# Performance work log

Measured on AMD Instinct MI355X. Metric: run time of the kernel, lower is better.

## Reference

```python
import jax, jax.numpy as jnp
import numpy as np

N = 20000      # nodes
E = 320000     # edges per timestep
T = 16         # timesteps
F_IN = 128     # node_features
F1, H1 = 64, 4 # gat1 filters/heads (concat=True)
F2, H2 = 64, 4 # gat2 filters/heads (concat=False -> mean over heads)
NEG_SLOPE = 0.2
EPS = 1e-16


def setup_inputs() -> dict:
    key = jax.random.key(0)
    ks = jax.random.split(key, 18)
    s = 0.05
    rn = lambda k, shp: (jax.random.normal(k, shp, jnp.float32) * s)
    return {
        "x_sequence": jax.random.normal(ks[0], (N, T, F_IN), jnp.float32),
        "edge_index_sequence": jax.random.randint(ks[1], (T, 2, E), 0, N, jnp.int32),
        # GATConv 1 (in=F_IN, out=F1, heads=H1, concat=True)
        "W1": rn(ks[2], (F_IN, H1 * F1)),
        "att_src1": rn(ks[3], (H1, F1)),
        "att_dst1": rn(ks[4], (H1, F1)),
        "b1": rn(ks[5], (H1 * F1,)),
        # GATConv 2 (in=H1*F1, out=F2, heads=H2, concat=False)
        "W2": rn(ks[6], (H1 * F1, H2 * F2)),
        "att_src2": rn(ks[7], (H2, F2)),
        "att_dst2": rn(ks[8], (H2, F2)),
        "b2": rn(ks[9], (F2,)),
        # GRU (input=F2, hidden=F2); layout: x @ W_ih + b_ih, gates [r|z|n]
        "W_ih": rn(ks[10], (F2, 3 * F2)),
        "W_hh": rn(ks[11], (F2, 3 * F2)),
        "b_ih": rn(ks[12], (3 * F2,)),
        "b_hh": rn(ks[13], (3 * F2,)),
        # final Linear(F2 -> 1)
        "W_out": rn(ks[14], (F2, 1)),
        "b_out": rn(ks[15], (1,)),
    }


def _gat(x, src, dst, W, a_src, a_dst, bias, heads, out_ch, concat):
    """PyG-style GATConv with self-loops already appended to (src, dst)."""
    n = x.shape[0]
    h = (x @ W).reshape(n, heads, out_ch)            # [N, H, C]
    al_src = jnp.einsum("nhc,hc->nh", h, a_src)       # [N, H]
    al_dst = jnp.einsum("nhc,hc->nh", h, a_dst)
    e = al_src[src] + al_dst[dst]                     # [E, H]
    e = jax.nn.leaky_relu(e, NEG_SLOPE)
    # segment softmax over edges grouped by destination node
    m = jax.ops.segment_max(e, dst, num_segments=n)   # [N, H]
    e = jnp.exp(e - m[dst])
    denom = jax.ops.segment_sum(e, dst, num_segments=n)
    alpha = e / (denom[dst] + EPS)                    # [E, H]
    msg = h[src] * alpha[:, :, None]                  # [E, H, C]
    out = jax.ops.segment_sum(msg, dst, num_segments=n)  # [N, H, C]
    out = out.reshape(n, heads * out_ch) if concat else out.mean(axis=1)
    return out + bias


def reference(x_sequence, edge_index_sequence, W1, att_src1, att_dst1, b1,
              W2, att_src2, att_dst2, b2, W_ih, W_hh, b_ih, b_hh, W_out, b_out):
    loops = jnp.arange(N, dtype=edge_index_sequence.dtype)

    def gat_step(_, inp):
        x_t, ei = inp                                 # [N,F_IN], [2,E]
        src = jnp.concatenate([ei[0], loops])         # add self-loops
        dst = jnp.concatenate([ei[1], loops])
        h = jax.nn.relu(_gat(x_t, src, dst, W1, att_src1, att_dst1, b1, H1, F1, True))
        h = jax.nn.relu(_gat(h, src, dst, W2, att_src2, att_dst2, b2, H2, F2, False))
        return None, h

    xs = (jnp.swapaxes(x_sequence, 0, 1), edge_index_sequence)  # [T,N,F_IN], [T,2,E]
    _, gat_out = jax.lax.scan(gat_step, None, xs)               # [T, N, F2]

    def gru_step(h_prev, x_t):
        gi = x_t @ W_ih + b_ih
        gh = h_prev @ W_hh + b_hh
        ir, iz, ig = jnp.split(gi, 3, axis=-1)
        hr, hz, hg = jnp.split(gh, 3, axis=-1)
        r = jax.nn.sigmoid(ir + hr)
        z = jax.nn.sigmoid(iz + hz)
        g = jnp.tanh(ig + r * hg)
        h = (1.0 - z) * g + z * h_prev
        return h, None

    h0 = jnp.zeros((N, F2), x_sequence.dtype)
    h_last, _ = jax.lax.scan(gru_step, h0, gat_out)             # [N, F2]
    return (h_last @ W_out + b_out).squeeze(-1)                  # [N]
```

## Files before the change

### kernel.cpp

```cpp
#include <hip/hip_runtime.h>
#include <math.h>

#define N_NODES 20000
#define N_EDGES 320000
#define T_STEPS 16
#define TB 8
#define RB_ROWS (N_NODES * TB)
#define F_INDIM 128
#define HC 256
#define HEADS 4
#define CDIM 64
#define G3 192
#define EPN (N_EDGES + N_NODES)
#define CSR_NB 20
#define CSR_EPB 16000

typedef __attribute__((ext_vector_type(8))) short bf16x8;
typedef __attribute__((ext_vector_type(8))) unsigned short ushort8;
typedef __attribute__((ext_vector_type(4))) float f32x4;
typedef __attribute__((ext_vector_type(4))) _Float16 half4;
typedef __attribute__((ext_vector_type(8))) _Float16 half8;

__device__ inline unsigned short f2bf(float x) {
    unsigned int u = __builtin_bit_cast(unsigned int, x);
    u += 0x7fffu + ((u >> 16) & 1u);
    return (unsigned short)(u >> 16);
}
__device__ inline void split_hilo(float x, unsigned short& h, unsigned short& l) {
    h = f2bf(x);
    float hf = __builtin_bit_cast(float, (unsigned int)h << 16);
    l = f2bf(x - hf);
}
__device__ inline ushort8 f4_to_hilo(float4 v) {
    ushort8 o;
    split_hilo(v.x, ((unsigned short*)&o)[0], ((unsigned short*)&o)[1]);
    split_hilo(v.y, ((unsigned short*)&o)[2], ((unsigned short*)&o)[3]);
    split_hilo(v.z, ((unsigned short*)&o)[4], ((unsigned short*)&o)[5]);
    split_hilo(v.w, ((unsigned short*)&o)[6], ((unsigned short*)&o)[7]);
    return o;
}
__device__ inline float fsig(float x) { return 1.f / (1.f + __expf(-x)); }
__device__ inline float ftanh(float x) {
    x = fminf(fmaxf(x, -15.f), 15.f);
    float e = __expf(2.f * x);
    return (e - 1.f) / (e + 1.f);
}


__global__ void k_wsplit(const float* __restrict__ W, unsigned short* __restrict__ Wt,
                         int K, int Ncol) {
    int idx = blockIdx.x * 256 + threadIdx.x;
    if (idx >= K * Ncol) return;
    int k = idx / Ncol, c = idx - k * Ncol;
    unsigned short h, l;
    split_hilo(W[idx], h, l);
    Wt[(size_t)c * 2 * K + 2 * k] = h;
    Wt[(size_t)c * 2 * K + 2 * k + 1] = l;
}

__global__ void k_whalf(const float* __restrict__ W, _Float16* __restrict__ Wt,
                        int K, int Ncol) {
    int idx = blockIdx.x * 256 + threadIdx.x;
    if (idx >= K * Ncol) return;
    int k = idx / Ncol, c = idx - k * Ncol;
    Wt[(size_t)c * K + k] = (_Float16)W[idx];
}


__global__ __launch_bounds__(1024) void k_csr_hist(const int* __restrict__ ei,
                                                   unsigned int* __restrict__ partial,
                                                   unsigned short* __restrict__ lrank16) {
    __shared__ unsigned int hist[N_NODES];
    const int t = blockIdx.y, b = blockIdx.x;
    const int tid = threadIdx.x;
    for (int i = tid; i < N_NODES; i += 1024) hist[i] = 0;
    __syncthreads();
    const int* dst = ei + (size_t)t * 2 * N_EDGES + N_EDGES;
    const int e1 = min(b * CSR_EPB + CSR_EPB, N_EDGES);
    for (int e = b * CSR_EPB + tid; e < e1; e += 1024) {
        unsigned int lr = atomicAdd(&hist[dst[e]], 1u);
        lrank16[(size_t)t * N_EDGES + e] = (unsigned short)lr;
    }
    __syncthreads();
    unsigned int* pp = partial + ((size_t)t * CSR_NB + b) * N_NODES;
    for (int i = tid; i < N_NODES; i += 1024) pp[i] = hist[i];
}

__global__ void k_csr_colscan(unsigned int* __restrict__ partial,
                              unsigned int* __restrict__ total) {
    int idx = blockIdx.x * 256 + threadIdx.x;
    if (idx >= T_STEPS * N_NODES) return;
    int t = idx / N_NODES;
    int d = idx - t * N_NODES;
    unsigned int* pb = partial + (size_t)t * CSR_NB * N_NODES + d;
    unsigned int acc = 0;
#pragma unroll
    for (int b = 0; b < CSR_NB; ++b) {
        unsigned int c = pb[(size_t)b * N_NODES];
        pb[(size_t)b * N_NODES] = acc;
        acc += c;
    }
    total[idx] = acc + 1;
}

__global__ __launch_bounds__(1024) void k_csr_scan(const unsigned int* __restrict__ total,
                                                   int* __restrict__ off_all,
                                                   unsigned short* __restrict__ csr16) {
    __shared__ int sdata[1024];
    const int t = blockIdx.x;
    const unsigned int* tot = total + (size_t)t * N_NODES;
    int* off = off_all + t * (N_NODES + 1);
    unsigned short* cs = csr16 + (size_t)t * EPN;
    const int tid = threadIdx.x;
    const int ITEMS = (N_NODES + 1023) / 1024;
    const int start = tid * ITEMS;
    int local = 0;
    for (int i = 0; i < ITEMS; ++i) {
        int d = start + i;
        if (d < N_NODES) local += tot[d];
    }
    sdata[tid] = local;
    __syncthreads();
    for (int s = 1; s < 1024; s <<= 1) {
        int v = (tid >= s) ? sdata[tid - s] : 0;
        __syncthreads();
        sdata[tid] += v;
        __syncthreads();
    }
    int run = sdata[tid] - local;
    for (int i = 0; i < ITEMS; ++i) {
        int d = start + i;
        if (d < N_NODES) {
            off[d] = run;
            cs[run] = (unsigned short)d;
            run += tot[d];
        }
    }
    if (tid == 0) off[N_NODES] = EPN;
}

__global__ void k_csr_fold(unsigned int* __restrict__ partial,
                           const int* __restrict__ off_all) {
    int idx = blockIdx.x * 256 + threadIdx.x;
    if (idx >= T_STEPS * CSR_NB * N_NODES) return;
    int t = idx / (CSR_NB * N_NODES);
    int rem = idx - t * (CSR_NB * N_NODES);
    int d = rem % N_NODES;
    partial[idx] += (unsigned int)(off_all[t * (N_NODES + 1) + d] + 1);
}

__global__ void k_csr_fill(const int* __restrict__ ei,
                           const unsigned int* __restrict__ partial,
                           const unsigned short* __restrict__ lrank16,
                           unsigned short* __restrict__ csr16) {
    const int bid = blockIdx.x;
    const int t = bid & 15;
    const int i = bid >> 4;
    const int e = i * 256 + threadIdx.x;
    const int* ep = ei + (size_t)t * 2 * N_EDGES;
    int s = ep[e], d = ep[N_EDGES + e];
    int b = e / CSR_EPB;
    unsigned int pos = partial[((size_t)t * CSR_NB + b) * N_NODES + d]
                     + lrank16[(size_t)t * N_EDGES + e];
    csr16[(size_t)t * EPN + pos] = (unsigned short)s;
}


template <bool XMAP, bool ATTN, bool CHALF, int BN, bool AF32, int DT>
__global__ __launch_bounds__(256) void k_gemm_mfma(const unsigned short* __restrict__ A, int lda,
                                                   const unsigned short* __restrict__ Bt,
                                                   float* __restrict__ C, int ldc,
                                                   int K2, int tbase,
                                                   const float* __restrict__ a_src,
                                                   const float* __restrict__ a_dst,
                                                   float* __restrict__ asb,
                                                   float* __restrict__ adb) {
    __shared__ unsigned short sA[128][40];
    __shared__ unsigned short sB[BN][40];
    const int NJ = BN / 16;
    const int tid = threadIdx.x;
    const int wid = tid >> 6, lane = tid & 63;
    const int row0 = blockIdx.y * 128;
    const int col0 = blockIdx.x * BN;

    const int ar = tid >> 1, aq = (tid & 1) * 8;
    const int bc = tid >> 2, bq = (tid & 3) * 8;

    int l = row0 + ar;
    int rg;
    if (XMAP) { int tl = l / N_NODES; int s = l - tl * N_NODES; rg = s * T_STEPS + tbase + tl; }
    else rg = l;
    const unsigned short* Arow = A + (size_t)rg * lda;
    const float* Arowf = (const float*)A + (size_t)rg * lda;
    const unsigned short* Brow = Bt + (size_t)(col0 + bc) * K2;
    const unsigned short* Brow2 = (BN == 128) ? (Bt + (size_t)(col0 + bc + 64) * K2) : Brow;

    const int fr = lane & 15;
    const int kg = lane >> 4;

    f32x4 acc[2][NJ] = {};

    for (int kk = 0; kk < K2; kk += 32) {
        ushort8 a0, a1;
        if (AF32) {
            float4 fa0 = *(const float4*)(Arowf + ((kk + aq) >> 1));
            float4 fa1 = *(const float4*)(Arowf + ((kk + aq) >> 1) + 8);
            a0 = f4_to_hilo(fa0);
            a1 = f4_to_hilo(fa1);
        } else {
            a0 = *(const ushort8*)(Arow + kk + aq);
            a1 = *(const ushort8*)(Arow + kk + aq + 16);
        }
        ushort8 b0 = *(const ushort8*)(Brow + kk + bq);
        ushort8 b1;
        if (BN == 128) b1 = *(const ushort8*)(Brow2 + kk + bq);
        *(ushort8*)&sA[ar][aq] = a0;
        *(ushort8*)&sA[ar][aq + 16] = a1;
        *(ushort8*)&sB[bc][bq] = b0;
        if (BN == 128) *(ushort8*)&sB[bc + 64][bq] = b1;
        __syncthreads();
        bf16x8 af[2], bfv[NJ];
#pragma unroll
        for (int i = 0; i < 2; ++i)
            af[i] = *(const bf16x8*)&sA[wid * 32 + i * 16 + fr][kg * 8];
#pragma unroll
        for (int j = 0; j < NJ; ++j)
            bfv[j] = *(const bf16x8*)&sB[j * 16 + fr][kg * 8];
#pragma unroll
        for (int i = 0; i < 2; ++i)
#pragma unroll
            for (int j = 0; j < NJ; ++j) {
                if (DT == 0)
                    acc[i][j] = __builtin_amdgcn_mfma_f32_16x16x32_bf16(af[i], bfv[j],
                                                                        acc[i][j], 0, 0, 0);
                else
                    acc[i][j] = __builtin_amdgcn_mfma_f32_16x16x32_f16(
                        __builtin_bit_cast(half8, af[i]), __builtin_bit_cast(half8, bfv[j]),
                        acc[i][j], 0, 0, 0);
            }
        __syncthreads();
    }
#pragma unroll
    for (int i = 0; i < 2; ++i)
#pragma unroll
        for (int j = 0; j < NJ; ++j) {
            int col = col0 + j * 16 + fr;
#pragma unroll
            for (int r = 0; r < 4; ++r) {
                int row = row0 + wid * 32 + i * 16 + kg * 4 + r;
                if (CHALF) {
                    _Float16* Ch = (_Float16*)C;
                    Ch[(size_t)row * ldc + col] = (_Float16)acc[i][j][r];
                } else {
                    C[(size_t)row * ldc + col] = acc[i][j][r];
                }
            }
        }

    if (ATTN) {
#pragma unroll
        for (int half = 0; half < BN / 64; ++half) {
            const int h_idx = (col0 >> 6) + half;
            float wa[4], wb[4];
#pragma unroll
            for (int j = 0; j < 4; ++j) {
                wa[j] = a_src[h_idx * 64 + j * 16 + fr];
                wb[j] = a_dst[h_idx * 64 + j * 16 + fr];
            }
#pragma unroll
            for (int i = 0; i < 2; ++i)
#pragma unroll
                for (int r = 0; r < 4; ++r) {
                    float sa = 0.f, sd = 0.f;
#pragma unroll
                    for (int j = 0; j < 4; ++j) {
                        sa = fmaf(acc[i][half * 4 + j][r], wa[j], sa);
                        sd = fmaf(acc[i][half * 4 + j][r], wb[j], sd);
                    }
#pragma unroll
                    for (int s = 1; s <= 8; s <<= 1) {
                        sa += __shfl_xor(sa, s, 64);
                        sd += __shfl_xor(sd, s, 64);
                    }
                    if (fr == 0) {
                        int row = row0 + wid * 32 + i * 16 + kg * 4 + r;
                        asb[(size_t)row * 4 + h_idx] = sa;
                        adb[(size_t)row * 4 + h_idx] = sd;
                    }
                }
        }
    }
}


template <bool CONCAT>
__global__ __launch_bounds__(256) void k_agg(const _Float16* __restrict__ hfeat,
                                             const float* __restrict__ asb,
                                             const float* __restrict__ adb,
                                             const int* __restrict__ off_all,
                                             const unsigned short* __restrict__ csr16,
                                             const float* __restrict__ bias,
                                             _Float16* __restrict__ out, int tbase) {
    const int bid = blockIdx.x;
    const int tl = bid & 7;
    const int nb = bid >> 3;
    const int t = tbase + tl;
    const int wid = threadIdx.x >> 6;
    const int d = nb * 4 + wid;
    const int lane = threadIdx.x & 63;
    const int h = lane >> 4;
    const int e16 = lane & 15;
    const int* off = off_all + (size_t)t * (N_NODES + 1);
    const int beg = off[d];
    const int deg = off[d + 1] - beg;
    const unsigned short* cs = csr16 + (size_t)t * EPN + beg;
    const float* asl = asb + (size_t)tl * N_NODES * HEADS;
    const half4* feat = (const half4*)(hfeat + (size_t)tl * N_NODES * HC) + lane;
    const float adh = adb[((size_t)tl * N_NODES + d) * HEADS + h];

    float ax = 0.f, ay = 0.f, az = 0.f, aw = 0.f, dlane = 0.f;
    const int widx = (lane & 48);

    int sreg = 0;
    float araw = 0.f;
    if (e16 < deg) {
        sreg = cs[e16];
        araw = asl[sreg * 4 + h];
    }

    for (int base = 0; base < deg; base += 16) {
        float wme = 0.f;
        if (base + e16 < deg) {
            float sc = araw + adh;
            sc = sc > 0.f ? sc : 0.2f * sc;
            wme = __expf(sc);
        }
        dlane += wme;

        int nxt = base + 16;
        int sregN = 0;
        float arawN = 0.f;
        if (nxt + e16 < deg) {
            sregN = cs[nxt + e16];
            arawN = asl[sregN * 4 + h];
        }

        const int len = min(16, deg - base);
        int q = 0;
        for (; q + 4 <= len; q += 4) {
#pragma unroll
            for (int u = 0; u < 4; ++u) {
                int qq = q + u;
                float wq = __shfl(wme, widx | qq, 64);
                int sq = __builtin_amdgcn_readlane(sreg, qq);
                half4 v = feat[(size_t)sq * 64];
                ax = fmaf(wq, (float)v[0], ax);
                ay = fmaf(wq, (float)v[1], ay);
                az = fmaf(wq, (float)v[2], az);
                aw = fmaf(wq, (float)v[3], aw);
            }
        }
        for (; q < len; ++q) {
            float wq = __shfl(wme, widx | q, 64);
            int sq = __builtin_amdgcn_readlane(sreg, q);
            half4 v = feat[(size_t)sq * 64];
            ax = fmaf(wq, (float)v[0], ax);
            ay = fmaf(wq, (float)v[1], ay);
            az = fmaf(wq, (float)v[2], az);
            aw = fmaf(wq, (float)v[3], aw);
        }
        sreg = sregN;
        araw = arawN;
    }
    float denom = dlane;
#pragma unroll
    for (int s = 1; s <= 8; s <<= 1) denom += __shfl_xor(denom, s, 64);
    float inv = 1.f / (denom + 1e-16f);
    ax *= inv; ay *= inv; az *= inv; aw *= inv;

    if (CONCAT) {
        float4 b = ((const float4*)bias)[lane];
        half4 o;
        o[0] = (_Float16)fmaxf(ax + b.x, 0.f);
        o[1] = (_Float16)fmaxf(ay + b.y, 0.f);
        o[2] = (_Float16)fmaxf(az + b.z, 0.f);
        o[3] = (_Float16)fmaxf(aw + b.w, 0.f);
        *(half4*)(out + ((size_t)tl * N_NODES + d) * HC + lane * 4) = o;
    } else {
        ax += __shfl_xor(ax, 16, 64); ax += __shfl_xor(ax, 32, 64);
        ay += __shfl_xor(ay, 16, 64); ay += __shfl_xor(ay, 32, 64);
        az += __shfl_xor(az, 16, 64); az += __shfl_xor(az, 32, 64);
        aw += __shfl_xor(aw, 16, 64); aw += __shfl_xor(aw, 32, 64);
        if (h == 0) {
            float4 b = ((const float4*)bias)[e16];
            half4 o;
            o[0] = (_Float16)fmaxf(ax * 0.25f + b.x, 0.f);
            o[1] = (_Float16)fmaxf(ay * 0.25f + b.y, 0.f);
            o[2] = (_Float16)fmaxf(az * 0.25f + b.z, 0.f);
            o[3] = (_Float16)fmaxf(aw * 0.25f + b.w, 0.f);
            *(half4*)(out + ((size_t)d * T_STEPS + t) * CDIM + e16 * 4) = o;
        }
    }
}


#define GRU_NPB 40
#define GRU_THREADS 512

__global__ __launch_bounds__(GRU_THREADS, 4) void k_gru_all(const _Float16* __restrict__ GI,
                                                            const float* __restrict__ Whh,
                                                            const float* __restrict__ bih,
                                                            const float* __restrict__ bhh,
                                                            const float* __restrict__ Wout,
                                                            const float* __restrict__ bout,
                                                            float* __restrict__ out) {
    __shared__ f32x4 sWp[16 * 3 * 64];
    __shared__ float sH[GRU_NPB][68];
    const int tid = threadIdx.x;
    const int c = tid & 63;
    const int ng = tid >> 6;
    const int n0 = ng * 5;
    const int nid0 = blockIdx.x * GRU_NPB + n0;

    for (int i = tid; i < 16 * 3 * 64; i += GRU_THREADS) {
        int k4 = i / 192, rem = i - k4 * 192;
        int pp = rem >> 6, cc = rem & 63;
        f32x4 w;
#pragma unroll
        for (int q = 0; q < 4; ++q) w[q] = Whh[(k4 * 4 + q) * G3 + pp * 64 + cc];
        sWp[i] = w;
    }
    for (int i = tid; i < GRU_NPB * 68; i += GRU_THREADS) ((float*)sH)[i] = 0.f;
    __syncthreads();

    const float bi0 = bih[c], bi1 = bih[64 + c], bi2 = bih[128 + c];
    const float bh0 = bhh[c], bh1 = bhh[64 + c], bh2 = bhh[128 + c];

    for (int t = 0; t < T_STEPS; ++t) {
        float gi0[5], gi1[5], gi2[5];
#pragma unroll
        for (int n = 0; n < 5; ++n) {
            const _Float16* gp = GI + ((size_t)(nid0 + n) * T_STEPS + t) * G3;
            gi0[n] = (float)gp[c]; gi1[n] = (float)gp[64 + c]; gi2[n] = (float)gp[128 + c];
        }
        float a0[5] = {}, a1[5] = {}, a2[5] = {};
#pragma unroll 4
        for (int k4 = 0; k4 < 16; ++k4) {
            f32x4 h4[5];
#pragma unroll
            for (int n = 0; n < 5; ++n) h4[n] = *(const f32x4*)&sH[n0 + n][k4 * 4];
            f32x4 w0 = sWp[(k4 * 3 + 0) * 64 + c];
            f32x4 w1 = sWp[(k4 * 3 + 1) * 64 + c];
            f32x4 w2 = sWp[(k4 * 3 + 2) * 64 + c];
#pragma unroll
            for (int q = 0; q < 4; ++q)
#pragma unroll
                for (int n = 0; n < 5; ++n) {
                    float hv = h4[n][q];
                    a0[n] = fmaf(hv, w0[q], a0[n]);
                    a1[n] = fmaf(hv, w1[q], a1[n]);
                    a2[n] = fmaf(hv, w2[q], a2[n]);
                }
        }
#pragma unroll
        for (int n = 0; n < 5; ++n) {
            float r = fsig(gi0[n] + bi0 + a0[n] + bh0);
            float z = fsig(gi1[n] + bi1 + a1[n] + bh1);
            float g = ftanh(gi2[n] + bi2 + r * (a2[n] + bh2));
            sH[n0 + n][c] = (1.f - z) * g + z * sH[n0 + n][c];
        }
    }

    float wc = Wout[c];
    float b0 = bout[0];
#pragma unroll
    for (int n = 0; n < 5; ++n) {
        float v = sH[n0 + n][c] * wc;
#pragma unroll
        for (int s = 32; s >= 1; s >>= 1) v += __shfl_xor(v, s, 64);
        if (c == 0) out[nid0 + n] = v + b0;
    }
}


extern "C" void kernel_launch(void* const* d_in, const int* in_sizes, int n_in,
                              void* d_out, int out_size, void* d_ws, size_t ws_size,
                              hipStream_t stream) {
    const float* x   = (const float*)d_in[0];
    const int*   ei  = (const int*)d_in[1];
    const float* W1  = (const float*)d_in[2];
    const float* as1 = (const float*)d_in[3];
    const float* ad1 = (const float*)d_in[4];
    const float* b1  = (const float*)d_in[5];
    const float* W2  = (const float*)d_in[6];
    const float* as2 = (const float*)d_in[7];
    const float* ad2 = (const float*)d_in[8];
    const float* b2  = (const float*)d_in[9];
    const float* Wih = (const float*)d_in[10];
    const float* Whh = (const float*)d_in[11];
    const float* bih = (const float*)d_in[12];
    const float* bhh = (const float*)d_in[13];
    const float* Wout = (const float*)d_in[14];
    const float* bout = (const float*)d_in[15];

    char* p = (char*)d_ws;
    _Float16* h_half = (_Float16*)p;  p += 81920000;
    _Float16* g1_f16 = (_Float16*)p;  p += 81920000;
    _Float16* g2_f16 = (_Float16*)p;  p += 40960000;
    _Float16* GI_all = (_Float16*)p;  p += 122880000;
    float* asb = (float*)p;  p += 2560000;
    float* adb = (float*)p;  p += 2560000;
    unsigned short* w1t = (unsigned short*)p;  p += 131072;
    _Float16* w2h = (_Float16*)p;  p += 131072;
    _Float16* wihh = (_Float16*)p;  p += 24576;
    int* off_all = (int*)p;  p += 1280064;
    unsigned short* csr16 = (unsigned short*)p;  p += 10880000;
    unsigned int* partial = (unsigned int*)p;  p += (size_t)T_STEPS * CSR_NB * N_NODES * 4;
    unsigned int* total = (unsigned int*)p;  p += (size_t)T_STEPS * N_NODES * 4;
    unsigned short* lrank16 = (unsigned short*)p;  p += (size_t)T_STEPS * N_EDGES * 2;

    dim3 thr(256);

    k_wsplit<<<(F_INDIM * HC + 255) / 256, thr, 0, stream>>>(W1, w1t, F_INDIM, HC);
    k_whalf<<<(HC * HC + 255) / 256, thr, 0, stream>>>(W2, w2h, HC, HC);
    k_whalf<<<(CDIM * G3 + 255) / 256, thr, 0, stream>>>(Wih, wihh, CDIM, G3);

    k_csr_hist<<<dim3(CSR_NB, T_STEPS), 1024, 0, stream>>>(ei, partial, lrank16);
    k_csr_colscan<<<(T_STEPS * N_NODES + 255) / 256, thr, 0, stream>>>(partial, total);
    k_csr_scan<<<T_STEPS, 1024, 0, stream>>>(total, off_all, csr16);
    k_csr_fold<<<(T_STEPS * CSR_NB * N_NODES + 255) / 256, thr, 0, stream>>>(partial, off_all);
    k_csr_fill<<<(N_EDGES / 256) * T_STEPS, thr, 0, stream>>>(ei, partial, lrank16, csr16);

    for (int hb = 0; hb < 2; ++hb) {
        const int tbase = hb * TB;
        k_gemm_mfma<true, true, true, 128, true, 0><<<dim3(2, RB_ROWS / 128), thr, 0, stream>>>(
            (const unsigned short*)x, F_INDIM, w1t, (float*)h_half, HC, 2 * F_INDIM, tbase,
            as1, ad1, asb, adb);
        k_agg<true><<<N_NODES / 4 * TB, thr, 0, stream>>>(
            h_half, asb, adb, off_all, csr16, b1, g1_f16, tbase);
        k_gemm_mfma<false, true, true, 128, false, 1><<<dim3(2, RB_ROWS / 128), thr, 0, stream>>>(
            (const unsigned short*)g1_f16, HC, (const unsigned short*)w2h, (float*)h_half, HC,
            HC, tbase, as2, ad2, asb, adb);
        k_agg<false><<<N_NODES / 4 * TB, thr, 0, stream>>>(
            h_half, asb, adb, off_all, csr16, b2, g2_f16, tbase);
    }

    k_gemm_mfma<false, false, true, 64, false, 1><<<dim3(3, N_NODES * T_STEPS / 128), thr, 0,
                                                    stream>>>(
        (const unsigned short*)g2_f16, CDIM, (const unsigned short*)wihh, (float*)GI_all, G3,
        CDIM, 0, nullptr, nullptr, nullptr, nullptr);

    k_gru_all<<<N_NODES / GRU_NPB, GRU_THREADS, 0, stream>>>(GI_all, Whh, bih, bhh, Wout, bout,
                                                            (float*)d_out);
}
```

Measured before the change: 1.174 ms.

## Split GAT aggregation per head across blocks, add separate head-mean kernel

The aggregation kernel changes from one wave per destination node covering all four heads to one wave per (node, head) pair. Each wave processes four edges at once, with 16 lanes covering the 64 channels, and reduces partial sums across lanes. The grid grows fourfold. The non-concat layer now writes per-head results to a scratch buffer, and a new small kernel averages the heads and applies bias and ReLU. The aim is more parallelism and shorter per-wave serial loops over edges, at the cost of re-reading CSR indices and attention scores per head, an extra kernel launch, and a full intermediate write and read for the second layer.

Result: slower. 2.100 ms (+78.8%).

```diff
diff --git a/kernel.cpp b/kernel.cpp
--- a/kernel.cpp
+++ b/kernel.cpp
@@ -294,113 +294,116 @@
 
 
 template <bool CONCAT>
-__global__ __launch_bounds__(256) void k_agg(const _Float16* __restrict__ hfeat,
-                                             const float* __restrict__ asb,
-                                             const float* __restrict__ adb,
-                                             const int* __restrict__ off_all,
-                                             const unsigned short* __restrict__ csr16,
-                                             const float* __restrict__ bias,
-                                             _Float16* __restrict__ out, int tbase) {
+__global__ __launch_bounds__(256) void k_aggq(const _Float16* __restrict__ hfeat,
+                                              const float* __restrict__ asb,
+                                              const float* __restrict__ adb,
+                                              const int* __restrict__ off_all,
+                                              const unsigned short* __restrict__ csr16,
+                                              const float* __restrict__ bias,
+                                              _Float16* __restrict__ out, int tbase) {
     const int bid = blockIdx.x;
     const int tl = bid & 7;
-    const int nb = bid >> 3;
+    const int rem = bid >> 3;
+    const int nb = rem % (N_NODES / 4);
+    const int q = rem / (N_NODES / 4);
     const int t = tbase + tl;
     const int wid = threadIdx.x >> 6;
     const int d = nb * 4 + wid;
     const int lane = threadIdx.x & 63;
-    const int h = lane >> 4;
-    const int e16 = lane & 15;
+    const int e4 = lane >> 4;
+    const int c16 = lane & 15;
+
     const int* off = off_all + (size_t)t * (N_NODES + 1);
     const int beg = off[d];
     const int deg = off[d + 1] - beg;
     const unsigned short* cs = csr16 + (size_t)t * EPN + beg;
     const float* asl = asb + (size_t)tl * N_NODES * HEADS;
-    const half4* feat = (const half4*)(hfeat + (size_t)tl * N_NODES * HC) + lane;
-    const float adh = adb[((size_t)tl * N_NODES + d) * HEADS + h];
+    const _Float16* feat = hfeat + (size_t)tl * N_NODES * HC + q * 64 + c16 * 4;
+    const float adh = adb[((size_t)tl * N_NODES + d) * HEADS + q];
 
     float ax = 0.f, ay = 0.f, az = 0.f, aw = 0.f, dlane = 0.f;
-    const int widx = (lane & 48);
 
     int sreg = 0;
     float araw = 0.f;
-    if (e16 < deg) {
-        sreg = cs[e16];
-        araw = asl[sreg * 4 + h];
-    }
-
-    for (int base = 0; base < deg; base += 16) {
+    if (e4 < deg) {
+        sreg = cs[e4];
+        araw = asl[sreg * 4 + q];
+    }
+
+    for (int base = 0; base < deg; base += 4) {
+        bool act = (base + e4 < deg);
         float wme = 0.f;
-        if (base + e16 < deg) {
+        if (act) {
             float sc = araw + adh;
             sc = sc > 0.f ? sc : 0.2f * sc;
             wme = __expf(sc);
         }
         dlane += wme;
 
-        int nxt = base + 16;
+        int nxt = base + 4;
         int sregN = 0;
         float arawN = 0.f;
-        if (nxt + e16 < deg) {
-            sregN = cs[nxt + e16];
-            arawN = asl[sregN * 4 + h];
-        }
-
-        const int len = min(16, deg - base);
-        int q = 0;
-        for (; q + 4 <= len; q += 4) {
-#pragma unroll
-            for (int u = 0; u < 4; ++u) {
-                int qq = q + u;
-                float wq = __shfl(wme, widx | qq, 64);
-                int sq = __builtin_amdgcn_readlane(sreg, qq);
-                half4 v = feat[(size_t)sq * 64];
-                ax = fmaf(wq, (float)v[0], ax);
-                ay = fmaf(wq, (float)v[1], ay);
-                az = fmaf(wq, (float)v[2], az);
-                aw = fmaf(wq, (float)v[3], aw);
-            }
-        }
-        for (; q < len; ++q) {
-            float wq = __shfl(wme, widx | q, 64);
-            int sq = __builtin_amdgcn_readlane(sreg, q);
-            half4 v = feat[(size_t)sq * 64];
-            ax = fmaf(wq, (float)v[0], ax);
-            ay = fmaf(wq, (float)v[1], ay);
-            az = fmaf(wq, (float)v[2], az);
-            aw = fmaf(wq, (float)v[3], aw);
+        if (nxt + e4 < deg) {
+            sregN = cs[nxt + e4];
+            arawN = asl[sregN * 4 + q];
+        }
+
+        if (act) {
+            half4 v = *(const half4*)(feat + (size_t)sreg * HC);
+            ax = fmaf(wme, (float)v[0], ax);
+            ay = fmaf(wme, (float)v[1], ay);
+            az = fmaf(wme, (float)v[2], az);
+            aw = fmaf(wme, (float)v[3], aw);
         }
         sreg = sregN;
         araw = arawN;
     }
+
+    ax += __shfl_xor(ax, 16, 64); ax += __shfl_xor(ax, 32, 64);
+    ay += __shfl_xor(ay, 16, 64); ay += __shfl_xor(ay, 32, 64);
+    az += __shfl_xor(az, 16, 64); az += __shfl_xor(az, 32, 64);
+    aw += __shfl_xor(aw, 16, 64); aw += __shfl_xor(aw, 32, 64);
     float denom = dlane;
-#pragma unroll
-    for (int s = 1; s <= 8; s <<= 1) denom += __shfl_xor(denom, s, 64);
+    denom += __shfl_xor(denom, 16, 64); denom += __shfl_xor(denom, 32, 64);
     float inv = 1.f / (denom + 1e-16f);
     ax *= inv; ay *= inv; az *= inv; aw *= inv;
 
-    if (CONCAT) {
-        float4 b = ((const float4*)bias)[lane];
+    if (e4 == 0) {
         half4 o;
-        o[0] = (_Float16)fmaxf(ax + b.x, 0.f);
-        o[1] = (_Float16)fmaxf(ay + b.y, 0.f);
-        o[2] = (_Float16)fmaxf(az + b.z, 0.f);
-        o[3] = (_Float16)fmaxf(aw + b.w, 0.f);
-        *(half4*)(out + ((size_t)tl * N_NODES + d) * HC + lane * 4) = o;
-    } else {
-        ax += __shfl_xor(ax, 16, 64); ax += __shfl_xor(ax, 32, 64);
-        ay += __shfl_xor(ay, 16, 64); ay += __shfl_xor(ay, 32, 64);
-        az += __shfl_xor(az, 16, 64); az += __shfl_xor(az, 32, 64);
-        aw += __shfl_xor(aw, 16, 64); aw += __shfl_xor(aw, 32, 64);
-        if (h == 0) {
-            float4 b = ((const float4*)bias)[e16];
-            half4 o;
-            o[0] = (_Float16)fmaxf(ax * 0.25f + b.x, 0.f);
-            o[1] = (_Float16)fmaxf(ay * 0.25f + b.y, 0.f);
-            o[2] = (_Float16)fmaxf(az * 0.25f + b.z, 0.f);
-            o[3] = (_Float16)fmaxf(aw * 0.25f + b.w, 0.f);
-            *(half4*)(out + ((size_t)d * T_STEPS + t) * CDIM + e16 * 4) = o;
-        }
-    }
+        if (CONCAT) {
+            float4 b = ((const float4*)bias)[q * 16 + c16];
+            o[0] = (_Float16)fmaxf(ax + b.x, 0.f);
+            o[1] = (_Float16)fmaxf(ay + b.y, 0.f);
+            o[2] = (_Float16)fmaxf(az + b.z, 0.f);
+            o[3] = (_Float16)fmaxf(aw + b.w, 0.f);
+        } else {
+            o[0] = (_Float16)ax; o[1] = (_Float16)ay;
+            o[2] = (_Float16)az; o[3] = (_Float16)aw;
+        }
+        *(half4*)(out + ((size_t)tl * N_NODES + d) * HC + q * 64 + c16 * 4) = o;
+    }
+}
+
+__global__ void k_aggmean(const _Float16* __restrict__ valq, const float* __restrict__ bias,
+                          _Float16* __restrict__ g2, int tbase) {
+    int idx = blockIdx.x * 256 + threadIdx.x;
+    if (idx >= TB * N_NODES * 16) return;
+    int c16 = idx & 15;
+    int rem = idx >> 4;
+    int d = rem % N_NODES;
+    int tl = rem / N_NODES;
+    const _Float16* vp = valq + ((size_t)tl * N_NODES + d) * HC + c16 * 4;
+    half4 v0 = *(const half4*)(vp);
+    half4 v1 = *(const half4*)(vp + 64);
+    half4 v2 = *(const half4*)(vp + 128);
+    half4 v3 = *(const half4*)(vp + 192);
+    float4 b = ((const float4*)bias)[c16];
+    half4 o;
+    o[0] = (_Float16)fmaxf(0.25f * ((float)v0[0] + (float)v1[0] + (float)v2[0] + (float)v3[0]) + b.x, 0.f);
+    o[1] = (_Float16)fmaxf(0.25f * ((float)v0[1] + (float)v1[1] + (float)v2[1] + (float)v3[1]) + b.y, 0.f);
+    o[2] = (_Float16)fmaxf(0.25f * ((float)v0[2] + (float)v1[2] + (float)v2[2] + (float)v3[2]) + b.z, 0.f);
+    o[3] = (_Float16)fmaxf(0.25f * ((float)v0[3] + (float)v1[3] + (float)v2[3] + (float)v3[3]) + b.w, 0.f);
+    *(half4*)(g2 + ((size_t)d * T_STEPS + tbase + tl) * CDIM + c16 * 4) = o;
 }
 
 
@@ -520,6 +523,7 @@
     unsigned short* lrank16 = (unsigned short*)p;  p += (size_t)T_STEPS * N_EDGES * 2;
 
     dim3 thr(256);
+    const int AGGQ_GRID = HEADS * (N_NODES / 4) * 8;
 
     k_wsplit<<<(F_INDIM * HC + 255) / 256, thr, 0, stream>>>(W1, w1t, F_INDIM, HC);
     k_whalf<<<(HC * HC + 255) / 256, thr, 0, stream>>>(W2, w2h, HC, HC);
@@ -536,13 +540,14 @@
         k_gemm_mfma<true, true, true, 128, true, 0><<<dim3(2, RB_ROWS / 128), thr, 0, stream>>>(
             (const unsigned short*)x, F_INDIM, w1t, (float*)h_half, HC, 2 * F_INDIM, tbase,
             as1, ad1, asb, adb);
-        k_agg<true><<<N_NODES / 4 * TB, thr, 0, stream>>>(
+        k_aggq<true><<<AGGQ_GRID, thr, 0, stream>>>(
             h_half, asb, adb, off_all, csr16, b1, g1_f16, tbase);
         k_gemm_mfma<false, true, true, 128, false, 1><<<dim3(2, RB_ROWS / 128), thr, 0, stream>>>(
             (const unsigned short*)g1_f16, HC, (const unsigned short*)w2h, (float*)h_half, HC,
             HC, tbase, as2, ad2, asb, adb);
-        k_agg<false><<<N_NODES / 4 * TB, thr, 0, stream>>>(
-            h_half, asb, adb, off_all, csr16, b2, g2_f16, tbase);
+        k_aggq<false><<<AGGQ_GRID, thr, 0, stream>>>(
+            h_half, asb, adb, off_all, csr16, nullptr, g1_f16, tbase);
+        k_aggmean<<<(TB * N_NODES * 16 + 255) / 256, thr, 0, stream>>>(g1_f16, b2, g2_f16, tbase);
     }
 
     k_gemm_mfma<false, false, true, 64, false, 1><<<dim3(3, N_NODES * T_STEPS / 128), thr, 0,
```
